# Kernel optimization log

Measured on AMD Instinct MI355X. Metric: run time of the kernel, lower is better.

Reference implementation:

```python
import jax, jax.numpy as jnp
import numpy as np

B = 1048576
VEC_SZ = 4
LUT_BITS = 8
K = 2 ** LUT_BITS  # 256 codewords


def setup_inputs() -> dict:
    key = jax.random.key(0)
    kx, kt = jax.random.split(key)
    X = jax.random.normal(kx, (B, VEC_SZ), dtype=jnp.float32)
    tlut = jax.random.normal(kt, (K, VEC_SZ), dtype=jnp.float32)  # codebook [K, vec_sz]
    return {"X": X, "tlut": tlut}


def reference(X, tlut):
    # torch.cdist(X, tlut) -> argmin is equivalent to argmin of squared distances:
    x_sq = jnp.sum(X * X, axis=-1, keepdims=True)            # [B, 1]
    c_sq = jnp.sum(tlut * tlut, axis=-1)                     # [K]
    cross = jnp.einsum('bd,kd->bk', X, tlut)                 # [B, K]
    dist2 = x_sq - 2.0 * cross + c_sq                        # [B, K]
    state = jnp.argmin(dist2, axis=-1).astype(jnp.int32)     # [B]
    hatX = jnp.take(tlut, state, axis=0)                     # gather reconstruction [B, vec_sz]
    return hatX, state
```

## Files before the change

### kernel.cpp

```cpp
#include <hip/hip_runtime.h>

#define K_CW 256

__global__ void vq_csq_kernel(const float* __restrict__ tlut, float* __restrict__ csq) {
    int k = threadIdx.x;
    float c0 = tlut[k * 4 + 0];
    float c1 = tlut[k * 4 + 1];
    float c2 = tlut[k * 4 + 2];
    float c3 = tlut[k * 4 + 3];
    float s = __fadd_rn(__fadd_rn(__fadd_rn(__fmul_rn(c0, c0), __fmul_rn(c1, c1)),
                                  __fmul_rn(c2, c2)),
                        __fmul_rn(c3, c3));
    csq[k] = s;
}

__device__ __forceinline__ float dist2_ref(float x0, float x1, float x2, float x3,
                                           float xsq, float4 c, float cs) {
    float cross = __fmul_rn(x0, c.x);
    cross = __fmaf_rn(x1, c.y, cross);
    cross = __fmaf_rn(x2, c.z, cross);
    cross = __fmaf_rn(x3, c.w, cross);
    float t = __fmaf_rn(-2.0f, cross, xsq);
    return __fadd_rn(t, cs);
}

__global__ __launch_bounds__(256) void vq_argmin_kernel(
    const float* __restrict__ X,
    const float* __restrict__ tlut,
    const float* __restrict__ csq,
    float* __restrict__ outX,
    float* __restrict__ outS,
    int B) {
    int p = blockIdx.x * blockDim.x + threadIdx.x;
    if (p >= B) return;

    const float4 xv = reinterpret_cast<const float4*>(X)[p];
    const float x0 = xv.x, x1 = xv.y, x2 = xv.z, x3 = xv.w;

    float xsq = __fadd_rn(__fadd_rn(__fadd_rn(__fmul_rn(x0, x0), __fmul_rn(x1, x1)),
                                    __fmul_rn(x2, x2)),
                          __fmul_rn(x3, x3));

    float bestd = __builtin_inff();
    int besti = 0;

    #pragma unroll 4
    for (int k = 0; k < K_CW; k += 2) {
        const float4 ca = reinterpret_cast<const float4*>(tlut)[k];
        const float4 cb = reinterpret_cast<const float4*>(tlut)[k + 1];
        float da = dist2_ref(x0, x1, x2, x3, xsq, ca, csq[k]);
        float db = dist2_ref(x0, x1, x2, x3, xsq, cb, csq[k + 1]);
        if (da < bestd) { bestd = da; besti = k; }
        if (db < bestd) { bestd = db; besti = k + 1; }
    }

    const float4 cw = reinterpret_cast<const float4*>(tlut)[besti];
    reinterpret_cast<float4*>(outX)[p] = cw;
    outS[p] = (float)besti;
}

extern "C" void kernel_launch(void* const* d_in, const int* in_sizes, int n_in,
                              void* d_out, int out_size, void* d_ws, size_t ws_size,
                              hipStream_t stream) {
    const float* X    = (const float*)d_in[0];
    const float* tlut = (const float*)d_in[1];
    const int B = in_sizes[0] / 4;

    float* outX = (float*)d_out;
    float* outS = outX + (size_t)B * 4;

    float* csq = (float*)d_ws;

    vq_csq_kernel<<<1, 256, 0, stream>>>(tlut, csq);

    const int block = 256;
    const int grid = (B + block - 1) / block;
    vq_argmin_kernel<<<grid, block, 0, stream>>>(X, tlut, csq, outX, outS, B);
}
```

Baseline: 129.8 us.

## Process four points per thread to amortize codebook loads across points

Each thread now handles four points spaced B/4 apart and reuses each codebook entry and its squared norm across all four distance computations. The argmin update uses branchless selects instead of branches. This cuts per-point scalar codebook loads and loop overhead, but raises register use and cuts the thread count by four. It also assumes B is divisible by four, since leftover points would not be processed.

```diff
diff --git a/kernel.cpp b/kernel.cpp
--- a/kernel.cpp
+++ b/kernel.cpp
@@ -1,6 +1,7 @@
 #include <hip/hip_runtime.h>
 
 #define K_CW 256
+#define PPT 4
 
 __global__ void vq_csq_kernel(const float* __restrict__ tlut, float* __restrict__ csq) {
     int k = threadIdx.x;
@@ -14,16 +15,6 @@
     csq[k] = s;
 }
 
-__device__ __forceinline__ float dist2_ref(float x0, float x1, float x2, float x3,
-                                           float xsq, float4 c, float cs) {
-    float cross = __fmul_rn(x0, c.x);
-    cross = __fmaf_rn(x1, c.y, cross);
-    cross = __fmaf_rn(x2, c.z, cross);
-    cross = __fmaf_rn(x3, c.w, cross);
-    float t = __fmaf_rn(-2.0f, cross, xsq);
-    return __fadd_rn(t, cs);
-}
-
 __global__ __launch_bounds__(256) void vq_argmin_kernel(
     const float* __restrict__ X,
     const float* __restrict__ tlut,
@@ -31,32 +22,51 @@
     float* __restrict__ outX,
     float* __restrict__ outS,
     int B) {
-    int p = blockIdx.x * blockDim.x + threadIdx.x;
-    if (p >= B) return;
+    const int tid = blockIdx.x * blockDim.x + threadIdx.x;
+    const int stride = B / PPT;
+    if (tid >= stride) return;
 
-    const float4 xv = reinterpret_cast<const float4*>(X)[p];
-    const float x0 = xv.x, x1 = xv.y, x2 = xv.z, x3 = xv.w;
+    const float4* __restrict__ X4 = reinterpret_cast<const float4*>(X);
+    const float4* __restrict__ T4 = reinterpret_cast<const float4*>(tlut);
 
-    float xsq = __fadd_rn(__fadd_rn(__fadd_rn(__fmul_rn(x0, x0), __fmul_rn(x1, x1)),
-                                    __fmul_rn(x2, x2)),
-                          __fmul_rn(x3, x3));
+    float x0[PPT], x1[PPT], x2[PPT], x3[PPT], xsq[PPT], bestd[PPT];
+    int besti[PPT];
 
-    float bestd = __builtin_inff();
-    int besti = 0;
+    #pragma unroll
+    for (int i = 0; i < PPT; ++i) {
+        const float4 xv = X4[tid + i * stride];
+        x0[i] = xv.x; x1[i] = xv.y; x2[i] = xv.z; x3[i] = xv.w;
+        xsq[i] = __fadd_rn(__fadd_rn(__fadd_rn(__fmul_rn(xv.x, xv.x), __fmul_rn(xv.y, xv.y)),
+                                     __fmul_rn(xv.z, xv.z)),
+                           __fmul_rn(xv.w, xv.w));
+        bestd[i] = __builtin_inff();
+        besti[i] = 0;
+    }
 
     #pragma unroll 4
-    for (int k = 0; k < K_CW; k += 2) {
-        const float4 ca = reinterpret_cast<const float4*>(tlut)[k];
-        const float4 cb = reinterpret_cast<const float4*>(tlut)[k + 1];
-        float da = dist2_ref(x0, x1, x2, x3, xsq, ca, csq[k]);
-        float db = dist2_ref(x0, x1, x2, x3, xsq, cb, csq[k + 1]);
-        if (da < bestd) { bestd = da; besti = k; }
-        if (db < bestd) { bestd = db; besti = k + 1; }
+    for (int k = 0; k < K_CW; ++k) {
+        const float4 c = T4[k];
+        const float cs = csq[k];
+        #pragma unroll
+        for (int i = 0; i < PPT; ++i) {
+            float cross = __fmul_rn(x0[i], c.x);
+            cross = __fmaf_rn(x1[i], c.y, cross);
+            cross = __fmaf_rn(x2[i], c.z, cross);
+            cross = __fmaf_rn(x3[i], c.w, cross);
+            float t = __fmaf_rn(-2.0f, cross, xsq[i]);
+            float d = __fadd_rn(t, cs);
+            bool lt = d < bestd[i];
+            besti[i] = lt ? k : besti[i];
+            bestd[i] = lt ? d : bestd[i];
+        }
     }
 
-    const float4 cw = reinterpret_cast<const float4*>(tlut)[besti];
-    reinterpret_cast<float4*>(outX)[p] = cw;
-    outS[p] = (float)besti;
+    #pragma unroll
+    for (int i = 0; i < PPT; ++i) {
+        const int p = tid + i * stride;
+        reinterpret_cast<float4*>(outX)[p] = T4[besti[i]];
+        outS[p] = (float)besti[i];
+    }
 }
 
 extern "C" void kernel_launch(void* const* d_in, const int* in_sizes, int n_in,
@@ -73,7 +83,8 @@
 
     vq_csq_kernel<<<1, 256, 0, stream>>>(tlut, csq);
 
+    const int threads = B / PPT;
     const int block = 256;
-    const int grid = (B + block - 1) / block;
+    const int grid = (threads + block - 1) / block;
     vq_argmin_kernel<<<grid, block, 0, stream>>>(X, tlut, csq, outX, outS, B);
 }
```

Result: faster. 119.8 us (-7.7%).
